# Performance work log

Hardware: AMD Instinct MI355X
Metric: run time of the kernel (lower is better)

The kernel has to match this reference:

```python
import jax, jax.numpy as jnp
import numpy as np

NUM_HEADS = 32
NUM_KV_HEADS = 8
HEAD_DIM = 128
SCALE = 0.08838834764831845  # 1/sqrt(128)
NUM_SEQS = 8
Q_LEN = 256            # new tokens per sequence (uniform cu_seqlens_q)
MAX_PAGES = 128
PAGE_SIZE = 16
BLOCK_SIZE = 32
NUM_PAGES = NUM_SEQS * MAX_PAGES


def setup_inputs() -> dict:
    key = jax.random.key(0)
    ks = jax.random.split(key, 6)
    total = NUM_SEQS * Q_LEN
    q = jax.random.normal(ks[0], (total, NUM_HEADS * HEAD_DIM), dtype=jnp.float32)
    k = jax.random.normal(ks[1], (total, NUM_KV_HEADS * HEAD_DIM), dtype=jnp.float32)
    v = jax.random.normal(ks[2], (total, NUM_KV_HEADS * HEAD_DIM), dtype=jnp.float32)
    k_cache = jax.random.normal(ks[3], (NUM_PAGES, PAGE_SIZE, NUM_KV_HEADS, HEAD_DIM), dtype=jnp.float32)
    v_cache = jax.random.normal(ks[4], (NUM_PAGES, PAGE_SIZE, NUM_KV_HEADS, HEAD_DIM), dtype=jnp.float32)
    page_tables = jnp.arange(NUM_SEQS * MAX_PAGES, dtype=jnp.int32).reshape(NUM_SEQS, MAX_PAGES)
    context_lens = jax.random.randint(ks[5], (NUM_SEQS,), 0, MAX_PAGES * PAGE_SIZE, dtype=jnp.int32)
    return {
        'q': q, 'k': k, 'v': v,
        'k_cache': k_cache, 'v_cache': v_cache,
        'page_tables': page_tables, 'context_lens': context_lens,
        'page_size': PAGE_SIZE, 'block_size': BLOCK_SIZE,
    }


def reference(q, k, v, k_cache, v_cache, page_tables, context_lens, page_size, block_size):
    B, P = page_tables.shape
    S = q.shape[0] // B
    C = P * page_size                      # max cached context per seq
    G = NUM_HEADS // NUM_KV_HEADS          # GQA group size

    qb = q.reshape(B, S, NUM_KV_HEADS, G, HEAD_DIM)
    kb = k.reshape(B, S, NUM_KV_HEADS, HEAD_DIM)
    vb = v.reshape(B, S, NUM_KV_HEADS, HEAD_DIM)

    # page-table gather of cached K/V: [B, P, page_size, nkvh, hd] -> [B, C, nkvh, hd]
    k_ctx = k_cache[page_tables].reshape(B, C, NUM_KV_HEADS, HEAD_DIM)
    v_ctx = v_cache[page_tables].reshape(B, C, NUM_KV_HEADS, HEAD_DIM)

    k_full = jnp.concatenate([k_ctx, kb], axis=1)  # [B, C+S, nkvh, hd]
    v_full = jnp.concatenate([v_ctx, vb], axis=1)

    T = C + S
    t_idx = jnp.arange(T)
    s_idx = jnp.arange(S)
    # cached positions valid iff t < context_len; new positions use block mask
    ctx_valid = t_idx[None, :] < context_lens[:, None]            # [B, T]
    block_ends = (s_idx // block_size + 1) * block_size           # [S]
    new_valid = block_ends[:, None] > (t_idx[None, :] - C)        # [S, T]
    is_ctx = t_idx < C                                            # [T]
    mask = jnp.where(is_ctx[None, None, :], ctx_valid[:, None, :], new_valid[None, :, :])  # [B, S, T]

    # scores: [B, nkvh, G, S, T]
    scores = jnp.einsum('bsngd,btnd->bngst', qb, k_full) * SCALE
    scores = jnp.where(mask[:, None, None, :, :], scores, jnp.float32(-1e30))
    probs = jax.nn.softmax(scores, axis=-1)
    out = jnp.einsum('bngst,btnd->bsngd', probs, v_full)          # [B, S, nkvh, G, hd]
    return out.reshape(B * S, NUM_HEADS * HEAD_DIM)
```

## Files before the change

kernel.cpp:

```cpp
#include <hip/hip_runtime.h>
#include <hip/hip_bf16.h>

#define NUM_HEADS   32
#define NUM_KV_HEADS 8
#define HEAD_DIM    128
#define GQA          4
#define Q_LEN      256
#define MAX_PAGES  128
#define PAGE_SIZE   16
#define SCALE 0.08838834764831845f
#define LOG2E 1.44269504088896340736f
#define RESCALE_THR 8.0f

#define NCH_MAX   36
#define CHUNK_B   16384
#define KSTREAM   ((size_t)NCH_MAX * CHUNK_B)
#define NITEMS    512
#define PBYTES    33792

typedef __bf16 bf16x8 __attribute__((ext_vector_type(8)));
typedef float  f32x4  __attribute__((ext_vector_type(4)));

union B8 { uint4 u; bf16x8 v; };

__device__ __forceinline__ unsigned f2bf(float x){
    unsigned u = __builtin_bit_cast(unsigned, x);
    return (u + 0x7fffu + ((u >> 16) & 1u)) >> 16;
}
__device__ __forceinline__ unsigned pack2(float lo, float hi){
    return f2bf(lo) | (f2bf(hi) << 16);
}
__device__ __forceinline__ float bflo(unsigned h){
    return __builtin_bit_cast(float, h << 16);
}
__device__ __forceinline__ float bfhi(unsigned h){
    return __builtin_bit_cast(float, h & 0xffff0000u);
}

typedef __attribute__((address_space(3))) unsigned char lds_as3_t;
typedef const __attribute__((address_space(1))) void gas_v;
typedef __attribute__((address_space(3))) void las_v;

#define GLD16(g, l) __builtin_amdgcn_global_load_lds((gas_v*)(g), (las_v*)(l), 16, 0, 0)

#define TRR(dst, base, OFF) asm volatile("ds_read_b64_tr_b16 %0, %1 offset:" OFF \
                                         : "=v"(dst) : "v"(base))

__global__ __launch_bounds__(256) void prep_kernel(
    const float* __restrict__ knew,
    const float* __restrict__ vnew,
    const float* __restrict__ kcache,
    const float* __restrict__ vcache,
    const int*   __restrict__ ptab,
    const int*   __restrict__ ctxlens,
    unsigned char* __restrict__ kimg,
    unsigned char* __restrict__ vimg)
{
    const int ch  = blockIdx.x;
    const int kvh = blockIdx.y;
    const int b   = blockIdx.z;
    const int ctxlen = ctxlens[b];
    const int lim = ctxlen + Q_LEN;
    const int base = ch * 64;
    if (base >= lim) return;

    const int tid  = threadIdx.x;
    const int srow = tid >> 2;
    const int seg  = tid & 3;
    const int t    = base + srow;

    unsigned char* kdst = kimg + (size_t)(b * 8 + kvh) * KSTREAM + (size_t)ch * CHUNK_B;
    unsigned char* vdst = vimg + (size_t)(b * 8 + kvh) * KSTREAM + (size_t)ch * CHUNK_B;
    const int swz    = (srow & 7) << 4;
    const int vbyte0 = (srow >> 2) * 128 + (srow & 3) * 32;

    if (t < lim){
        size_t roff;
        const float *ksrc, *vsrc;
        if (t < ctxlen){
            const int page = ptab[b * MAX_PAGES + (t >> 4)];
            roff = ((size_t)(page * PAGE_SIZE + (t & 15)) * NUM_KV_HEADS + kvh) * HEAD_DIM;
            ksrc = kcache + roff; vsrc = vcache + roff;
        } else {
            roff = ((size_t)(b * Q_LEN + (t - ctxlen)) * NUM_KV_HEADS + kvh) * HEAD_DIM;
            ksrc = knew + roff; vsrc = vnew + roff;
        }
        const float* kr = ksrc + seg * 32;
        const float* vr = vsrc + seg * 32;
        #pragma unroll
        for (int i = 0; i < 4; ++i){
            float4 a  = *(const float4*)(kr + i * 8);
            float4 c4 = *(const float4*)(kr + i * 8 + 4);
            uint4 wv;
            wv.x = pack2(a.x, a.y);  wv.y = pack2(a.z, a.w);
            wv.z = pack2(c4.x, c4.y); wv.w = pack2(c4.z, c4.w);
            *(uint4*)(kdst + srow * 256 + ((seg * 64 + i * 16) ^ swz)) = wv;
        }
        #pragma unroll
        for (int db = 0; db < 2; ++db){
            const float4 a0 = *(const float4*)(vr + db * 16 + 0);
            const float4 a1 = *(const float4*)(vr + db * 16 + 4);
            const float4 a2 = *(const float4*)(vr + db * 16 + 8);
            const float4 a3 = *(const float4*)(vr + db * 16 + 12);
            uint4 w0, w1;
            w0.x = pack2(a0.x, a0.y); w0.y = pack2(a0.z, a0.w);
            w0.z = pack2(a1.x, a1.y); w0.w = pack2(a1.z, a1.w);
            w1.x = pack2(a2.x, a2.y); w1.y = pack2(a2.z, a2.w);
            w1.z = pack2(a3.x, a3.y); w1.w = pack2(a3.z, a3.w);
            const int dbk = seg * 2 + db;
            *(uint4*)(vdst + dbk * 2048 + vbyte0)      = w0;
            *(uint4*)(vdst + dbk * 2048 + vbyte0 + 16) = w1;
        }
    } else {
        const uint4 z = {0u, 0u, 0u, 0u};
        #pragma unroll
        for (int i = 0; i < 4; ++i)
            *(uint4*)(kdst + srow * 256 + ((seg * 64 + i * 16) ^ swz)) = z;
        #pragma unroll
        for (int db = 0; db < 2; ++db){
            const int dbk = seg * 2 + db;
            *(uint4*)(vdst + dbk * 2048 + vbyte0)      = z;
            *(uint4*)(vdst + dbk * 2048 + vbyte0 + 16) = z;
        }
    }
}

template<int NSPLIT>
__global__ __launch_bounds__(256, 2) void attn_kernel(
    const float* __restrict__ q,
    const int*   __restrict__ ctxlens,
    float*       __restrict__ out,
    const unsigned char* __restrict__ kimg,
    const unsigned char* __restrict__ vimg,
    unsigned char* __restrict__ part)
{
    __shared__ __align__(16) unsigned char lds[65536];

    const int tid  = threadIdx.x;
    const int w    = tid >> 6;
    const int lane = tid & 63;
    const int hh   = lane >> 4;
    const int cq   = lane & 15;

    const unsigned ldsb3 = (unsigned)(unsigned long long)(lds_as3_t*)(&lds[0]);

    const int fid   = blockIdx.x;
    const int item0 = fid / NSPLIT;
    const int seg   = fid % NSPLIT;

    const int b   = item0 & 7;
    const int kvh = (item0 >> 3) & 7;
    const int s32 = 7 - (item0 >> 6);

    const int s0 = s32 * 32;
    const int ctxlen = ctxlens[b];
    const int vlim = ctxlen + (s32 + 1) * 32;
    const int nch  = (vlim + 63) >> 6;
    const int lo   = (seg * nch) / NSPLIT;
    const int hi   = ((seg + 1) * nch) / NSPLIT;
    if (lo >= hi) return;
    const int hq = kvh * GQA + w;

    const unsigned char* kstream = kimg + (size_t)(b * 8 + kvh) * KSTREAM;
    const unsigned char* vstream = vimg + (size_t)(b * 8 + kvh) * KSTREAM;

    #define STAGE(CH, PB) do { \
        const unsigned char* kg_ = kstream + (size_t)(CH) * CHUNK_B + (w * 4096 + lane * 16); \
        const unsigned char* vg_ = vstream + (size_t)(CH) * CHUNK_B + (w * 4096 + lane * 16); \
        _Pragma("unroll") \
        for (int i_ = 0; i_ < 4; ++i_){ \
            GLD16(kg_ + i_ * 1024, lds + (PB) * CHUNK_B + w * 4096 + i_ * 1024); \
            GLD16(vg_ + i_ * 1024, lds + 32768 + (PB) * CHUNK_B + w * 4096 + i_ * 1024); \
        } \
    } while (0)

    STAGE(lo, lo & 1);

    B8 qf[2][4];
    #pragma unroll
    for (int u = 0; u < 2; ++u){
        const float* qrow = q + (size_t)(b * Q_LEN + s0 + u * 16 + cq) * (NUM_HEADS * HEAD_DIM)
                              + hq * HEAD_DIM;
        #pragma unroll
        for (int c = 0; c < 4; ++c){
            const float4 f0 = *(const float4*)(qrow + c * 32 + 8 * hh);
            const float4 f1 = *(const float4*)(qrow + c * 32 + 8 * hh + 4);
            const float sc = SCALE * LOG2E;
            qf[u][c].u.x = pack2(f0.x * sc, f0.y * sc);
            qf[u][c].u.y = pack2(f0.z * sc, f0.w * sc);
            qf[u][c].u.z = pack2(f1.x * sc, f1.y * sc);
            qf[u][c].u.w = pack2(f1.z * sc, f1.w * sc);
        }
    }

    f32x4 acc[2][8] = {};
    float mrun[2] = {-1e30f, -1e30f};
    float lp[2]   = {0.f, 0.f};

    __syncthreads();

    for (int ch = lo; ch < hi; ++ch){
        const int pb = ch & 1;
        if (ch + 1 < hi) STAGE(ch + 1, pb ^ 1);

        const int base = ch * 64;
        const unsigned kb = (unsigned)(pb * CHUNK_B);

        __builtin_amdgcn_s_setprio(1);
        f32x4 st[2][4] = {};
        #pragma unroll
        for (int c = 0; c < 4; ++c){
            #pragma unroll
            for (int tf = 0; tf < 4; ++tf){
                const int trow = tf * 16 + cq;
                const unsigned byte = kb + trow * 256 + ((c * 64 + hh * 16) ^ ((trow & 7) << 4));
                B8 kf; kf.u = *(const uint4*)(lds + byte);
                st[0][tf] = __builtin_amdgcn_mfma_f32_16x16x32_bf16(kf.v, qf[0][c].v, st[0][tf], 0, 0, 0);
                st[1][tf] = __builtin_amdgcn_mfma_f32_16x16x32_bf16(kf.v, qf[1][c].v, st[1][tf], 0, 0, 0);
            }
        }
        __builtin_amdgcn_s_setprio(0);

        B8 af[2][2];
        const bool interior = (base + 64 <= vlim);
        #pragma unroll
        for (int u = 0; u < 2; ++u){
            float p[4][4];
            float pm = -1e30f;
            if (interior){
                #pragma unroll
                for (int tf = 0; tf < 4; ++tf){
                    #pragma unroll
                    for (int r = 0; r < 4; ++r){
                        const float s = st[u][tf][r];
                        p[tf][r] = s;
                        pm = fmaxf(pm, s);
                    }
                }
            } else {
                #pragma unroll
                for (int tf = 0; tf < 4; ++tf){
                    #pragma unroll
                    for (int r = 0; r < 4; ++r){
                        const int t = base + tf * 16 + hh * 4 + r;
                        const float s = (t < vlim) ? st[u][tf][r] : -1e30f;
                        p[tf][r] = s;
                        pm = fmaxf(pm, s);
                    }
                }
            }
            pm = fmaxf(pm, __shfl_xor(pm, 16));
            pm = fmaxf(pm, __shfl_xor(pm, 32));

            if (!__all(pm <= mrun[u] + RESCALE_THR)){
                const float mnew  = fmaxf(mrun[u], pm);
                const float alpha = __builtin_amdgcn_exp2f(mrun[u] - mnew);
                mrun[u] = mnew;
                lp[u] *= alpha;
                float a4[4];
                #pragma unroll
                for (int r = 0; r < 4; ++r) a4[r] = __shfl(alpha, hh * 20 + r);
                #pragma unroll
                for (int dc = 0; dc < 8; ++dc){
                    #pragma unroll
                    for (int r = 0; r < 4; ++r) acc[u][dc][r] *= a4[r];
                }
            }
            const float m = mrun[u];
            float rsum = 0.f;
            #pragma unroll
            for (int tf = 0; tf < 4; ++tf){
                #pragma unroll
                for (int r = 0; r < 4; ++r){
                    const float e = __builtin_amdgcn_exp2f(p[tf][r] - m);
                    p[tf][r] = e;
                    rsum += e;
                }
            }
            lp[u] += rsum;

            unsigned pk01[4], pk23[4];
            #pragma unroll
            for (int tf = 0; tf < 4; ++tf){
                pk01[tf] = pack2(p[tf][0], p[tf][1]);
                pk23[tf] = pack2(p[tf][2], p[tf][3]);
            }
            af[u][0].u.x = pk01[0]; af[u][0].u.y = pk23[0]; af[u][0].u.z = pk01[1]; af[u][0].u.w = pk23[1];
            af[u][1].u.x = pk01[2]; af[u][1].u.y = pk23[2]; af[u][1].u.z = pk01[3]; af[u][1].u.w = pk23[3];
        }

        {
            const unsigned trb = ldsb3 + 32768u + (unsigned)(pb * CHUNK_B) + (unsigned)(hh * 128 + cq * 8);
            unsigned long long r0,r1,r2,r3,r4,r5,r6,r7;
            B8 vf;
            __builtin_amdgcn_s_setprio(1);
            TRR(r0, trb, "0");     TRR(r1, trb, "512");
            TRR(r2, trb, "2048");  TRR(r3, trb, "2560");
            TRR(r4, trb, "4096");  TRR(r5, trb, "4608");
            TRR(r6, trb, "6144");  TRR(r7, trb, "6656");
            asm volatile("s_waitcnt lgkmcnt(0)" ::: "memory");
            __builtin_amdgcn_sched_barrier(0);
            vf.u.x=(unsigned)r0; vf.u.y=(unsigned)(r0>>32); vf.u.z=(unsigned)r1; vf.u.w=(unsigned)(r1>>32);
            acc[0][0] = __builtin_amdgcn_mfma_f32_16x16x32_bf16(af[0][0].v, vf.v, acc[0][0], 0, 0, 0);
            acc[1][0] = __builtin_amdgcn_mfma_f32_16x16x32_bf16(af[1][0].v, vf.v, acc[1][0], 0, 0, 0);
            vf.u.x=(unsigned)r2; vf.u.y=(unsigned)(r2>>32); vf.u.z=(unsigned)r3; vf.u.w=(unsigned)(r3>>32);
            acc[0][1] = __builtin_amdgcn_mfma_f32_16x16x32_bf16(af[0][0].v, vf.v, acc[0][1], 0, 0, 0);
            acc[1][1] = __builtin_amdgcn_mfma_f32_16x16x32_bf16(af[1][0].v, vf.v, acc[1][1], 0, 0, 0);
            vf.u.x=(unsigned)r4; vf.u.y=(unsigned)(r4>>32); vf.u.z=(unsigned)r5; vf.u.w=(unsigned)(r5>>32);
            acc[0][2] = __builtin_amdgcn_mfma_f32_16x16x32_bf16(af[0][0].v, vf.v, acc[0][2], 0, 0, 0);
            acc[1][2] = __builtin_amdgcn_mfma_f32_16x16x32_bf16(af[1][0].v, vf.v, acc[1][2], 0, 0, 0);
            vf.u.x=(unsigned)r6; vf.u.y=(unsigned)(r6>>32); vf.u.z=(unsigned)r7; vf.u.w=(unsigned)(r7>>32);
            acc[0][3] = __builtin_amdgcn_mfma_f32_16x16x32_bf16(af[0][0].v, vf.v, acc[0][3], 0, 0, 0);
            acc[1][3] = __builtin_amdgcn_mfma_f32_16x16x32_bf16(af[1][0].v, vf.v, acc[1][3], 0, 0, 0);
            TRR(r0, trb, "8192");  TRR(r1, trb, "8704");
            TRR(r2, trb, "10240"); TRR(r3, trb, "10752");
            TRR(r4, trb, "12288"); TRR(r5, trb, "12800");
            TRR(r6, trb, "14336"); TRR(r7, trb, "14848");
            asm volatile("s_waitcnt lgkmcnt(0)" ::: "memory");
            __builtin_amdgcn_sched_barrier(0);
            vf.u.x=(unsigned)r0; vf.u.y=(unsigned)(r0>>32); vf.u.z=(unsigned)r1; vf.u.w=(unsigned)(r1>>32);
            acc[0][4] = __builtin_amdgcn_mfma_f32_16x16x32_bf16(af[0][0].v, vf.v, acc[0][4], 0, 0, 0);
            acc[1][4] = __builtin_amdgcn_mfma_f32_16x16x32_bf16(af[1][0].v, vf.v, acc[1][4], 0, 0, 0);
            vf.u.x=(unsigned)r2; vf.u.y=(unsigned)(r2>>32); vf.u.z=(unsigned)r3; vf.u.w=(unsigned)(r3>>32);
            acc[0][5] = __builtin_amdgcn_mfma_f32_16x16x32_bf16(af[0][0].v, vf.v, acc[0][5], 0, 0, 0);
            acc[1][5] = __builtin_amdgcn_mfma_f32_16x16x32_bf16(af[1][0].v, vf.v, acc[1][5], 0, 0, 0);
            vf.u.x=(unsigned)r4; vf.u.y=(unsigned)(r4>>32); vf.u.z=(unsigned)r5; vf.u.w=(unsigned)(r5>>32);
            acc[0][6] = __builtin_amdgcn_mfma_f32_16x16x32_bf16(af[0][0].v, vf.v, acc[0][6], 0, 0, 0);
            acc[1][6] = __builtin_amdgcn_mfma_f32_16x16x32_bf16(af[1][0].v, vf.v, acc[1][6], 0, 0, 0);
            vf.u.x=(unsigned)r6; vf.u.y=(unsigned)(r6>>32); vf.u.z=(unsigned)r7; vf.u.w=(unsigned)(r7>>32);
            acc[0][7] = __builtin_amdgcn_mfma_f32_16x16x32_bf16(af[0][0].v, vf.v, acc[0][7], 0, 0, 0);
            acc[1][7] = __builtin_amdgcn_mfma_f32_16x16x32_bf16(af[1][0].v, vf.v, acc[1][7], 0, 0, 0);
            TRR(r0, trb, "1024");  TRR(r1, trb, "1536");
            TRR(r2, trb, "3072");  TRR(r3, trb, "3584");
            TRR(r4, trb, "5120");  TRR(r5, trb, "5632");
            TRR(r6, trb, "7168");  TRR(r7, trb, "7680");
            asm volatile("s_waitcnt lgkmcnt(0)" ::: "memory");
            __builtin_amdgcn_sched_barrier(0);
            vf.u.x=(unsigned)r0; vf.u.y=(unsigned)(r0>>32); vf.u.z=(unsigned)r1; vf.u.w=(unsigned)(r1>>32);
            acc[0][0] = __builtin_amdgcn_mfma_f32_16x16x32_bf16(af[0][1].v, vf.v, acc[0][0], 0, 0, 0);
            acc[1][0] = __builtin_amdgcn_mfma_f32_16x16x32_bf16(af[1][1].v, vf.v, acc[1][0], 0, 0, 0);
            vf.u.x=(unsigned)r2; vf.u.y=(unsigned)(r2>>32); vf.u.z=(unsigned)r3; vf.u.w=(unsigned)(r3>>32);
            acc[0][1] = __builtin_amdgcn_mfma_f32_16x16x32_bf16(af[0][1].v, vf.v, acc[0][1], 0, 0, 0);
            acc[1][1] = __builtin_amdgcn_mfma_f32_16x16x32_bf16(af[1][1].v, vf.v, acc[1][1], 0, 0, 0);
            vf.u.x=(unsigned)r4; vf.u.y=(unsigned)(r4>>32); vf.u.z=(unsigned)r5; vf.u.w=(unsigned)(r5>>32);
            acc[0][2] = __builtin_amdgcn_mfma_f32_16x16x32_bf16(af[0][1].v, vf.v, acc[0][2], 0, 0, 0);
            acc[1][2] = __builtin_amdgcn_mfma_f32_16x16x32_bf16(af[1][1].v, vf.v, acc[1][2], 0, 0, 0);
            vf.u.x=(unsigned)r6; vf.u.y=(unsigned)(r6>>32); vf.u.z=(unsigned)r7; vf.u.w=(unsigned)(r7>>32);
            acc[0][3] = __builtin_amdgcn_mfma_f32_16x16x32_bf16(af[0][1].v, vf.v, acc[0][3], 0, 0, 0);
            acc[1][3] = __builtin_amdgcn_mfma_f32_16x16x32_bf16(af[1][1].v, vf.v, acc[1][3], 0, 0, 0);
            TRR(r0, trb, "9216");  TRR(r1, trb, "9728");
            TRR(r2, trb, "11264"); TRR(r3, trb, "11776");
            TRR(r4, trb, "13312"); TRR(r5, trb, "13824");
            TRR(r6, trb, "15360"); TRR(r7, trb, "15872");
            asm volatile("s_waitcnt lgkmcnt(0)" ::: "memory");
            __builtin_amdgcn_sched_barrier(0);
            vf.u.x=(unsigned)r0; vf.u.y=(unsigned)(r0>>32); vf.u.z=(unsigned)r1; vf.u.w=(unsigned)(r1>>32);
            acc[0][4] = __builtin_amdgcn_mfma_f32_16x16x32_bf16(af[0][1].v, vf.v, acc[0][4], 0, 0, 0);
            acc[1][4] = __builtin_amdgcn_mfma_f32_16x16x32_bf16(af[1][1].v, vf.v, acc[1][4], 0, 0, 0);
            vf.u.x=(unsigned)r2; vf.u.y=(unsigned)(r2>>32); vf.u.z=(unsigned)r3; vf.u.w=(unsigned)(r3>>32);
            acc[0][5] = __builtin_amdgcn_mfma_f32_16x16x32_bf16(af[0][1].v, vf.v, acc[0][5], 0, 0, 0);
            acc[1][5] = __builtin_amdgcn_mfma_f32_16x16x32_bf16(af[1][1].v, vf.v, acc[1][5], 0, 0, 0);
            vf.u.x=(unsigned)r4; vf.u.y=(unsigned)(r4>>32); vf.u.z=(unsigned)r5; vf.u.w=(unsigned)(r5>>32);
            acc[0][6] = __builtin_amdgcn_mfma_f32_16x16x32_bf16(af[0][1].v, vf.v, acc[0][6], 0, 0, 0);
            acc[1][6] = __builtin_amdgcn_mfma_f32_16x16x32_bf16(af[1][1].v, vf.v, acc[1][6], 0, 0, 0);
            vf.u.x=(unsigned)r6; vf.u.y=(unsigned)(r6>>32); vf.u.z=(unsigned)r7; vf.u.w=(unsigned)(r7>>32);
            acc[0][7] = __builtin_amdgcn_mfma_f32_16x16x32_bf16(af[0][1].v, vf.v, acc[0][7], 0, 0, 0);
            acc[1][7] = __builtin_amdgcn_mfma_f32_16x16x32_bf16(af[1][1].v, vf.v, acc[1][7], 0, 0, 0);
            __builtin_amdgcn_s_setprio(0);
        }
        __syncthreads();
    }

    if (NSPLIT == 1){
        #pragma unroll
        for (int u = 0; u < 2; ++u){
            float l = lp[u];
            l += __shfl_xor(l, 16);
            l += __shfl_xor(l, 32);
            const float li = 1.0f / l;
            float li4[4];
            #pragma unroll
            for (int r = 0; r < 4; ++r) li4[r] = __shfl(li, hh * 20 + r);
            #pragma unroll
            for (int dc = 0; dc < 8; ++dc){
                #pragma unroll
                for (int r = 0; r < 4; ++r){
                    const int so = s0 + u * 16 + hh * 4 + r;
                    out[(size_t)(b * Q_LEN + so) * (NUM_HEADS * HEAD_DIM) + hq * HEAD_DIM + dc * 16 + cq]
                        = acc[u][dc][r] * li4[r];
                }
            }
        }
    } else {
        unsigned char* pp = part + (size_t)fid * PBYTES;
        #pragma unroll
        for (int u = 0; u < 2; ++u){
            float l = lp[u];
            l += __shfl_xor(l, 16);
            l += __shfl_xor(l, 32);
            if (hh == 0){
                float2 ml; ml.x = mrun[u]; ml.y = l;
                *(float2*)(pp + 32768 + (size_t)(w * 32 + u * 16 + cq) * 8) = ml;
            }
            #pragma unroll
            for (int dc = 0; dc < 8; ++dc){
                uint2 pk;
                pk.x = pack2(acc[u][dc][0], acc[u][dc][1]);
                pk.y = pack2(acc[u][dc][2], acc[u][dc][3]);
                *(uint2*)(pp + (size_t)((((w * 2 + u) * 8 + dc) * 64 + lane)) * 8) = pk;
            }
        }
    }
    #undef STAGE
}

template<int NSPLIT>
__global__ __launch_bounds__(256) void merge_kernel(
    const int* __restrict__ ctxlens,
    const unsigned char* __restrict__ part,
    float* __restrict__ out)
{
    __shared__ float s_w[NSPLIT][128];

    const int item0 = blockIdx.x;
    const int b   = item0 & 7;
    const int kvh = (item0 >> 3) & 7;
    const int s32 = 7 - (item0 >> 6);
    const int vlim = ctxlens[b] + (s32 + 1) * 32;
    const int nch  = (vlim + 63) >> 6;

    const int tid = threadIdx.x;

    bool act[NSPLIT];
    #pragma unroll
    for (int s = 0; s < NSPLIT; ++s){
        const int lo = (s * nch) / NSPLIT;
        const int hi = ((s + 1) * nch) / NSPLIT;
        act[s] = hi > lo;
    }

    if (tid < 128){
        float m[NSPLIT], l[NSPLIT];
        float M = -1e30f;
        #pragma unroll
        for (int s = 0; s < NSPLIT; ++s){
            if (act[s]){
                const float2 ml = *(const float2*)(part + (size_t)(item0 * NSPLIT + s) * PBYTES
                                                   + 32768 + (size_t)tid * 8);
                m[s] = ml.x; l[s] = ml.y;
                M = fmaxf(M, m[s]);
            }
        }
        float L = 0.f;
        float wg[NSPLIT];
        #pragma unroll
        for (int s = 0; s < NSPLIT; ++s){
            if (act[s]){
                wg[s] = __builtin_amdgcn_exp2f(m[s] - M);
                L += l[s] * wg[s];
            } else wg[s] = 0.f;
        }
        const float inv = 1.0f / L;
        #pragma unroll
        for (int s = 0; s < NSPLIT; ++s) s_w[s][tid] = wg[s] * inv;
    }
    __syncthreads();

    for (int k = 0; k < 8; ++k){
        const int q4 = tid + k * 256;
        const int S0 = q4 * 2;
        const int g  = S0 >> 6;
        const int ln = S0 & 63;
        const int hD = g >> 4;
        const int u  = (g >> 3) & 1;
        const int dc = g & 7;
        const int hh = ln >> 4;
        const int cq = ln & 15;
        const int wbase = hD * 32 + u * 16 + hh * 4;

        float o0[4] = {0.f, 0.f, 0.f, 0.f};
        float o1[4] = {0.f, 0.f, 0.f, 0.f};
        #pragma unroll
        for (int s = 0; s < NSPLIT; ++s){
            if (!act[s]) continue;
            const uint4 v = *(const uint4*)(part + (size_t)(item0 * NSPLIT + s) * PBYTES
                                            + (size_t)q4 * 16);
            const float w0 = s_w[s][wbase + 0];
            const float w1 = s_w[s][wbase + 1];
            const float w2 = s_w[s][wbase + 2];
            const float w3 = s_w[s][wbase + 3];
            o0[0] += w0 * bflo(v.x); o0[1] += w1 * bfhi(v.x);
            o0[2] += w2 * bflo(v.y); o0[3] += w3 * bfhi(v.y);
            o1[0] += w0 * bflo(v.z); o1[1] += w1 * bfhi(v.z);
            o1[2] += w2 * bflo(v.w); o1[3] += w3 * bfhi(v.w);
        }
        float* obase = out + (size_t)(b * Q_LEN + s32 * 32 + u * 16 + hh * 4) * (NUM_HEADS * HEAD_DIM)
                     + (kvh * GQA + hD) * HEAD_DIM + dc * 16 + cq;
        #pragma unroll
        for (int r = 0; r < 4; ++r){
            float2 ov; ov.x = o0[r]; ov.y = o1[r];
            *(float2*)(obase + (size_t)r * (NUM_HEADS * HEAD_DIM)) = ov;
        }
    }
}

extern "C" void kernel_launch(void* const* d_in, const int* in_sizes, int n_in,
                              void* d_out, int out_size, void* d_ws, size_t ws_size,
                              hipStream_t stream) {
    const float* q  = (const float*)d_in[0];
    const float* k  = (const float*)d_in[1];
    const float* v  = (const float*)d_in[2];
    const float* kc = (const float*)d_in[3];
    const float* vc = (const float*)d_in[4];
    const int*   pt = (const int*)d_in[5];
    const int*   cl = (const int*)d_in[6];
    float* o = (float*)d_out;

    const size_t img_bytes = (size_t)64 * KSTREAM;
    const size_t off_part  = 256 + 2 * img_bytes;
    const size_t need2 = off_part + (size_t)NITEMS * 2 * PBYTES;
    const size_t need1 = off_part;

    unsigned char* kimg = (unsigned char*)d_ws + 256;
    unsigned char* vimg = kimg + img_bytes;
    unsigned char* part = (unsigned char*)d_ws + off_part;

    prep_kernel<<<dim3(NCH_MAX, 8, 8), 256, 0, stream>>>(k, v, kc, vc, pt, cl, kimg, vimg);

    if (ws_size >= need2) {
        attn_kernel<2><<<NITEMS * 2, 256, 0, stream>>>(q, cl, o, kimg, vimg, part);
        merge_kernel<2><<<NITEMS, 256, 0, stream>>>(cl, part, o);
    } else if (ws_size >= need1) {
        attn_kernel<1><<<NITEMS, 256, 0, stream>>>(q, cl, o, kimg, vimg, part);
    }
}
```

Baseline: 138.7 us.

## Process two 32-row query tiles per block with 512 threads to share KV staging

Each attention block now runs 8 waves covering 64 query rows (two 32-row tiles) per KV head, so each staged K/V chunk in LDS serves twice as many queries and the number of work items halves. Staging work is spread across 8 waves, and the partial buffer and merge kernel are resized to match. The cross-lane max shuffle now runs only when a rescale is needed, and masking uses -inf. The cost is that the shorter-causal tile iterates up to the longer tile's chunk count, with those extra chunks fully masked, and there are fewer blocks in total.

```diff
diff --git a/kernel.cpp b/kernel.cpp
--- a/kernel.cpp
+++ b/kernel.cpp
@@ -11,12 +11,13 @@
 #define SCALE 0.08838834764831845f
 #define LOG2E 1.44269504088896340736f
 #define RESCALE_THR 8.0f
+#define NEGINF (-__builtin_inff())
 
 #define NCH_MAX   36
 #define CHUNK_B   16384
 #define KSTREAM   ((size_t)NCH_MAX * CHUNK_B)
-#define NITEMS    512
-#define PBYTES    33792
+#define NITEMS    256
+#define PBYTES    67584
 
 typedef __bf16 bf16x8 __attribute__((ext_vector_type(8)));
 typedef float  f32x4  __attribute__((ext_vector_type(4)));
@@ -126,7 +127,7 @@
 }
 
 template<int NSPLIT>
-__global__ __launch_bounds__(256, 2) void attn_kernel(
+__global__ __launch_bounds__(512, 4) void attn_kernel(
     const float* __restrict__ q,
     const int*   __restrict__ ctxlens,
     float*       __restrict__ out,
@@ -137,10 +138,12 @@
     __shared__ __align__(16) unsigned char lds[65536];
 
     const int tid  = threadIdx.x;
-    const int w    = tid >> 6;
+    const int w8   = tid >> 6;
     const int lane = tid & 63;
     const int hh   = lane >> 4;
     const int cq   = lane & 15;
+    const int head = w8 & 3;
+    const int p    = w8 >> 2;
 
     const unsigned ldsb3 = (unsigned)(unsigned long long)(lds_as3_t*)(&lds[0]);
 
@@ -150,27 +153,28 @@
 
     const int b   = item0 & 7;
     const int kvh = (item0 >> 3) & 7;
-    const int s32 = 7 - (item0 >> 6);
-
-    const int s0 = s32 * 32;
+    const int g   = 3 - (item0 >> 6);
+
     const int ctxlen = ctxlens[b];
-    const int vlim = ctxlen + (s32 + 1) * 32;
-    const int nch  = (vlim + 63) >> 6;
+    const int vlim = ctxlen + (2 * g + p + 1) * 32;
+    const int vmax = ctxlen + (2 * g + 2) * 32;
+    const int nch  = (vmax + 63) >> 6;
     const int lo   = (seg * nch) / NSPLIT;
     const int hi   = ((seg + 1) * nch) / NSPLIT;
     if (lo >= hi) return;
-    const int hq = kvh * GQA + w;
+    const int hq  = kvh * GQA + head;
+    const int s0w = (2 * g + p) * 32;
 
     const unsigned char* kstream = kimg + (size_t)(b * 8 + kvh) * KSTREAM;
     const unsigned char* vstream = vimg + (size_t)(b * 8 + kvh) * KSTREAM;
 
     #define STAGE(CH, PB) do { \
-        const unsigned char* kg_ = kstream + (size_t)(CH) * CHUNK_B + (w * 4096 + lane * 16); \
-        const unsigned char* vg_ = vstream + (size_t)(CH) * CHUNK_B + (w * 4096 + lane * 16); \
+        const unsigned char* kg_ = kstream + (size_t)(CH) * CHUNK_B + (w8 * 1024 + lane * 16); \
+        const unsigned char* vg_ = vstream + (size_t)(CH) * CHUNK_B + (w8 * 1024 + lane * 16); \
         _Pragma("unroll") \
-        for (int i_ = 0; i_ < 4; ++i_){ \
-            GLD16(kg_ + i_ * 1024, lds + (PB) * CHUNK_B + w * 4096 + i_ * 1024); \
-            GLD16(vg_ + i_ * 1024, lds + 32768 + (PB) * CHUNK_B + w * 4096 + i_ * 1024); \
+        for (int i_ = 0; i_ < 2; ++i_){ \
+            GLD16(kg_ + i_ * 8192, lds + (PB) * 16384 + w8 * 1024 + i_ * 8192); \
+            GLD16(vg_ + i_ * 8192, lds + 32768 + (PB) * 16384 + w8 * 1024 + i_ * 8192); \
         } \
     } while (0)
 
@@ -179,7 +183,7 @@
     B8 qf[2][4];
     #pragma unroll
     for (int u = 0; u < 2; ++u){
-        const float* qrow = q + (size_t)(b * Q_LEN + s0 + u * 16 + cq) * (NUM_HEADS * HEAD_DIM)
+        const float* qrow = q + (size_t)(b * Q_LEN + s0w + u * 16 + cq) * (NUM_HEADS * HEAD_DIM)
                               + hq * HEAD_DIM;
         #pragma unroll
         for (int c = 0; c < 4; ++c){
@@ -204,7 +208,7 @@
         if (ch + 1 < hi) STAGE(ch + 1, pb ^ 1);
 
         const int base = ch * 64;
-        const unsigned kb = (unsigned)(pb * CHUNK_B);
+        const unsigned kb = (unsigned)(pb * 16384);
 
         __builtin_amdgcn_s_setprio(1);
         f32x4 st[2][4] = {};
@@ -225,16 +229,16 @@
         const bool interior = (base + 64 <= vlim);
         #pragma unroll
         for (int u = 0; u < 2; ++u){
-            float p[4][4];
-            float pm = -1e30f;
+            float pv[4][4];
+            float pml = NEGINF;
             if (interior){
                 #pragma unroll
                 for (int tf = 0; tf < 4; ++tf){
                     #pragma unroll
                     for (int r = 0; r < 4; ++r){
                         const float s = st[u][tf][r];
-                        p[tf][r] = s;
-                        pm = fmaxf(pm, s);
+                        pv[tf][r] = s;
+                        pml = fmaxf(pml, s);
                     }
                 }
             } else {
@@ -243,16 +247,15 @@
                     #pragma unroll
                     for (int r = 0; r < 4; ++r){
                         const int t = base + tf * 16 + hh * 4 + r;
-                        const float s = (t < vlim) ? st[u][tf][r] : -1e30f;
-                        p[tf][r] = s;
-                        pm = fmaxf(pm, s);
+                        const float s = (t < vlim) ? st[u][tf][r] : NEGINF;
+                        pv[tf][r] = s;
+                        pml = fmaxf(pml, s);
                     }
                 }
             }
-            pm = fmaxf(pm, __shfl_xor(pm, 16));
-            pm = fmaxf(pm, __shfl_xor(pm, 32));
-
-            if (!__all(pm <= mrun[u] + RESCALE_THR)){
+            if (!__all(pml <= mrun[u] + RESCALE_THR)){
+                float pm = fmaxf(pml, __shfl_xor(pml, 16));
+                pm = fmaxf(pm, __shfl_xor(pm, 32));
                 const float mnew  = fmaxf(mrun[u], pm);
                 const float alpha = __builtin_amdgcn_exp2f(mrun[u] - mnew);
                 mrun[u] = mnew;
@@ -272,8 +275,8 @@
             for (int tf = 0; tf < 4; ++tf){
                 #pragma unroll
                 for (int r = 0; r < 4; ++r){
-                    const float e = __builtin_amdgcn_exp2f(p[tf][r] - m);
-                    p[tf][r] = e;
+                    const float e = __builtin_amdgcn_exp2f(pv[tf][r] - m);
+                    pv[tf][r] = e;
                     rsum += e;
                 }
             }
@@ -282,15 +285,15 @@
             unsigned pk01[4], pk23[4];
             #pragma unroll
             for (int tf = 0; tf < 4; ++tf){
-                pk01[tf] = pack2(p[tf][0], p[tf][1]);
-                pk23[tf] = pack2(p[tf][2], p[tf][3]);
+                pk01[tf] = pack2(pv[tf][0], pv[tf][1]);
+                pk23[tf] = pack2(pv[tf][2], pv[tf][3]);
             }
             af[u][0].u.x = pk01[0]; af[u][0].u.y = pk23[0]; af[u][0].u.z = pk01[1]; af[u][0].u.w = pk23[1];
             af[u][1].u.x = pk01[2]; af[u][1].u.y = pk23[2]; af[u][1].u.z = pk01[3]; af[u][1].u.w = pk23[3];
         }
 
         {
-            const unsigned trb = ldsb3 + 32768u + (unsigned)(pb * CHUNK_B) + (unsigned)(hh * 128 + cq * 8);
+            const unsigned trb = ldsb3 + 32768u + (unsigned)(pb * 16384) + (unsigned)(hh * 128 + cq * 8);
             unsigned long long r0,r1,r2,r3,r4,r5,r6,r7;
             B8 vf;
             __builtin_amdgcn_s_setprio(1);
@@ -385,7 +388,7 @@
             for (int dc = 0; dc < 8; ++dc){
                 #pragma unroll
                 for (int r = 0; r < 4; ++r){
-                    const int so = s0 + u * 16 + hh * 4 + r;
+                    const int so = s0w + u * 16 + hh * 4 + r;
                     out[(size_t)(b * Q_LEN + so) * (NUM_HEADS * HEAD_DIM) + hq * HEAD_DIM + dc * 16 + cq]
                         = acc[u][dc][r] * li4[r];
                 }
@@ -400,14 +403,14 @@
             l += __shfl_xor(l, 32);
             if (hh == 0){
                 float2 ml; ml.x = mrun[u]; ml.y = l;
-                *(float2*)(pp + 32768 + (size_t)(w * 32 + u * 16 + cq) * 8) = ml;
+                *(float2*)(pp + 65536 + (size_t)(head * 64 + p * 32 + u * 16 + cq) * 8) = ml;
             }
             #pragma unroll
             for (int dc = 0; dc < 8; ++dc){
                 uint2 pk;
                 pk.x = pack2(acc[u][dc][0], acc[u][dc][1]);
                 pk.y = pack2(acc[u][dc][2], acc[u][dc][3]);
-                *(uint2*)(pp + (size_t)((((w * 2 + u) * 8 + dc) * 64 + lane)) * 8) = pk;
+                *(uint2*)(pp + (size_t)((((head * 4 + p * 2 + u) * 8 + dc) * 64 + lane)) * 8) = pk;
             }
         }
     }
@@ -420,14 +423,14 @@
     const unsigned char* __restrict__ part,
     float* __restrict__ out)
 {
-    __shared__ float s_w[NSPLIT][128];
+    __shared__ float s_w[NSPLIT][256];
 
     const int item0 = blockIdx.x;
     const int b   = item0 & 7;
     const int kvh = (item0 >> 3) & 7;
-    const int s32 = 7 - (item0 >> 6);
-    const int vlim = ctxlens[b] + (s32 + 1) * 32;
-    const int nch  = (vlim + 63) >> 6;
+    const int g   = 3 - (item0 >> 6);
+    const int vmax = ctxlens[b] + (2 * g + 2) * 32;
+    const int nch  = (vmax + 63) >> 6;
 
     const int tid = threadIdx.x;
 
@@ -439,14 +442,14 @@
         act[s] = hi > lo;
     }
 
-    if (tid < 128){
+    {
         float m[NSPLIT], l[NSPLIT];
-        float M = -1e30f;
+        float M = NEGINF;
         #pragma unroll
         for (int s = 0; s < NSPLIT; ++s){
             if (act[s]){
                 const float2 ml = *(const float2*)(part + (size_t)(item0 * NSPLIT + s) * PBYTES
-                                                   + 32768 + (size_t)tid * 8);
+                                                   + 65536 + (size_t)tid * 8);
                 m[s] = ml.x; l[s] = ml.y;
                 M = fmaxf(M, m[s]);
             }
@@ -466,17 +469,16 @@
     }
     __syncthreads();
 
-    for (int k = 0; k < 8; ++k){
+    for (int k = 0; k < 16; ++k){
         const int q4 = tid + k * 256;
-        const int S0 = q4 * 2;
-        const int g  = S0 >> 6;
-        const int ln = S0 & 63;
-        const int hD = g >> 4;
-        const int u  = (g >> 3) & 1;
-        const int dc = g & 7;
-        const int hh = ln >> 4;
-        const int cq = ln & 15;
-        const int wbase = hD * 32 + u * 16 + hh * 4;
+        const int gidx = q4 >> 5;
+        const int head = gidx >> 5;
+        const int t2   = (gidx >> 3) & 3;
+        const int dc   = gidx & 7;
+        const int ln   = (q4 * 2) & 63;
+        const int hh   = ln >> 4;
+        const int cq   = ln & 15;
+        const int wb   = head * 64 + t2 * 16 + hh * 4;
 
         float o0[4] = {0.f, 0.f, 0.f, 0.f};
         float o1[4] = {0.f, 0.f, 0.f, 0.f};
@@ -485,17 +487,17 @@
             if (!act[s]) continue;
             const uint4 v = *(const uint4*)(part + (size_t)(item0 * NSPLIT + s) * PBYTES
                                             + (size_t)q4 * 16);
-            const float w0 = s_w[s][wbase + 0];
-            const float w1 = s_w[s][wbase + 1];
-            const float w2 = s_w[s][wbase + 2];
-            const float w3 = s_w[s][wbase + 3];
+            const float w0 = s_w[s][wb + 0];
+            const float w1 = s_w[s][wb + 1];
+            const float w2 = s_w[s][wb + 2];
+            const float w3 = s_w[s][wb + 3];
             o0[0] += w0 * bflo(v.x); o0[1] += w1 * bfhi(v.x);
             o0[2] += w2 * bflo(v.y); o0[3] += w3 * bfhi(v.y);
             o1[0] += w0 * bflo(v.z); o1[1] += w1 * bfhi(v.z);
             o1[2] += w2 * bflo(v.w); o1[3] += w3 * bfhi(v.w);
         }
-        float* obase = out + (size_t)(b * Q_LEN + s32 * 32 + u * 16 + hh * 4) * (NUM_HEADS * HEAD_DIM)
-                     + (kvh * GQA + hD) * HEAD_DIM + dc * 16 + cq;
+        float* obase = out + (size_t)(b * Q_LEN + g * 64 + t2 * 16 + hh * 4) * (NUM_HEADS * HEAD_DIM)
+                     + (kvh * GQA + head) * HEAD_DIM + dc * 16 + cq;
         #pragma unroll
         for (int r = 0; r < 4; ++r){
             float2 ov; ov.x = o0[r]; ov.y = o1[r];
@@ -528,9 +530,9 @@
     prep_kernel<<<dim3(NCH_MAX, 8, 8), 256, 0, stream>>>(k, v, kc, vc, pt, cl, kimg, vimg);
 
     if (ws_size >= need2) {
-        attn_kernel<2><<<NITEMS * 2, 256, 0, stream>>>(q, cl, o, kimg, vimg, part);
+        attn_kernel<2><<<NITEMS * 2, 512, 0, stream>>>(q, cl, o, kimg, vimg, part);
         merge_kernel<2><<<NITEMS, 256, 0, stream>>>(cl, part, o);
     } else if (ws_size >= need1) {
-        attn_kernel<1><<<NITEMS, 256, 0, stream>>>(q, cl, o, kimg, vimg, part);
-    }
-}
+        attn_kernel<1><<<NITEMS, 512, 0, stream>>>(q, cl, o, kimg, vimg, part);
+    }
+}
```

Measured after the change: 206.9 us. 49.2% more time.
